# Kernel tuning notes

Measured on AMD Instinct MI355X. Metric: run time of the kernel, lower is better.

The kernel has to match this reference:

```python
import jax, jax.numpy as jnp
import numpy as np

N_IND, N_ORG, N_EXT = 1_000_000, 300_000, 100_000
F = 64
E = 1_000_000
# (src_type, dst_type) per relation, in HeteroConv dict order:
# txn: ind->ind, org->ind, ext->ind, ind->org, org->org, ext->org; role: ind->org;
# rev_txn: ind->ind, org->ind, ext->ind, ind->org, org->org, ext->org; rev_role: org->ind
RELS = [("ind","ind"),("org","ind"),("ext","ind"),("ind","org"),("org","org"),("ext","org"),
        ("ind","org"),("ind","ind"),("org","ind"),("ext","ind"),("ind","org"),("org","org"),
        ("ext","org"),("org","ind")]
N_OF = {"ind": N_IND, "org": N_ORG, "ext": N_EXT}


def setup_inputs() -> dict:
    key = jax.random.key(0)
    ks = jax.random.split(key, 8)
    x_ind = jax.random.normal(ks[0], (N_IND, F), dtype=jnp.float32)
    x_org = jax.random.normal(ks[1], (N_ORG, F), dtype=jnp.float32)
    x_ext = jax.random.normal(ks[2], (N_EXT, F), dtype=jnp.float32)
    Wl = jax.random.normal(ks[3], (14, F, 1), dtype=jnp.float32) * 0.1
    Wr = jax.random.normal(ks[4], (14, F, 1), dtype=jnp.float32) * 0.1
    b = jax.random.normal(ks[5], (14, 1), dtype=jnp.float32) * 0.1
    # Per-relation edge_index with src/dst ids in the correct node-count ranges.
    eis = []
    for r, (s, d) in enumerate(RELS):
        k1, k2 = jax.random.split(jax.random.fold_in(ks[6], r))
        src = jax.random.randint(k1, (E,), 0, N_OF[s], dtype=jnp.int32)
        dst = jax.random.randint(k2, (E,), 0, N_OF[d], dtype=jnp.int32)
        eis.append(jnp.stack([src, dst]))
    edge_index = jnp.stack(eis)  # [14, 2, E]
    return {"x_ind": x_ind, "x_org": x_org, "x_ext": x_ext,
            "Wl": Wl, "Wr": Wr, "b": b, "edge_index": edge_index}


def _segment_mean(feat, dst, num_segments):
    # PyG 'mean' aggr: zero for isolated dst nodes.
    s = jax.ops.segment_sum(feat, dst, num_segments=num_segments)          # [N_dst, F]
    c = jax.ops.segment_sum(jnp.ones((dst.shape[0], 1), feat.dtype), dst,
                            num_segments=num_segments)                      # [N_dst, 1]
    return s / jnp.maximum(c, 1.0)


def reference(x_ind, x_org, x_ext, Wl, Wr, b, edge_index):
    x = {"ind": x_ind, "org": x_org, "ext": x_ext}
    out = {"ind": jnp.zeros((N_IND, 1), x_ind.dtype),
           "org": jnp.zeros((N_ORG, 1), x_org.dtype)}
    for r, (s, d) in enumerate(RELS):
        src, dst = edge_index[r, 0], edge_index[r, 1]
        agg = _segment_mean(x[s][src], dst, N_OF[d])   # mean of neighbor feats [N_dst, F]
        # SAGEConv: lin_l(agg) + lin_r(x_dst); bias lives in lin_l. HeteroConv sums relations.
        out[d] = out[d] + agg @ Wl[r] + x[d] @ Wr[r] + b[r]
    pred_ind = jax.nn.sigmoid(out["ind"])[:, 0]
    pred_org = jax.nn.sigmoid(out["org"])[:, 0]
    return (pred_ind, pred_org)
```

## Files before the change

### kernel.cpp

```cpp
#include <hip/hip_runtime.h>
#include <hip/hip_fp16.h>

#define N_IND 1000000
#define N_ORG 300000
#define N_EXT 100000
#define F 64
#define E_PER 1000000
#define NREL 14

#define BW 1024
#define NB_IND 977
#define NB_ORG 293
#define NBKT 1270
#define NB_H 1024
#define CHUNK 4096
#define COLS_PER_REL 245
#define NCOL (NREL * COLS_PER_REL)
#define LAST_N (E_PER - (COLS_PER_REL - 1) * CHUNK)
#define COLS_PER_TYPE (7 * COLS_PER_REL)

#define FIX_SCALE 262144.0f
#define FIX_INV   3.814697265625e-6f

static const size_t OFF_PAY      = 0;
static const size_t OFF_CNTOFF   = 14049280;
static const size_t OFF_CNTOFF_T = 17561600;
static const size_t OFF_P_IND    = 21073920;
static const size_t OFF_P_ORG    = 23573920;
static const size_t OFF_P_EXT    = 24323920;
static const size_t OFF_BASE_IND = 24523920;
static const size_t OFF_BASE_ORG = 25523920;
static const size_t OFF_WM_IND   = 25823920;
static const size_t OFF_WM_ORG   = 25824304;
static const size_t OFF_WM_EXT   = 25824688;
static const size_t OFF_BSUM     = 25824944;

__global__ void prep_kernel(const float* __restrict__ Wl,
                            const float* __restrict__ Wr,
                            const float* __restrict__ b,
                            float* __restrict__ wm_ind,
                            float* __restrict__ wm_org,
                            float* __restrict__ wm_ext,
                            float* __restrict__ bsum) {
    int t = threadIdx.x;
    const int ind_wl[5] = {0, 3, 6, 7, 10};
    const int org_wl[5] = {1, 4, 8, 11, 13};
    const int ext_wl[4] = {2, 5, 9, 12};
    const int ind_r[7]  = {0, 1, 2, 7, 8, 9, 13};
    const int org_r[7]  = {3, 4, 5, 6, 10, 11, 12};
#pragma unroll
    for (int k = 0; k < 5; ++k) wm_ind[k * 64 + t] = Wl[ind_wl[k] * 64 + t];
#pragma unroll
    for (int k = 0; k < 5; ++k) wm_org[k * 64 + t] = Wl[org_wl[k] * 64 + t];
#pragma unroll
    for (int k = 0; k < 4; ++k) wm_ext[k * 64 + t] = Wl[ext_wl[k] * 64 + t];
    float si = 0.f, so = 0.f;
#pragma unroll
    for (int k = 0; k < 7; ++k) {
        si += Wr[ind_r[k] * 64 + t];
        so += Wr[org_r[k] * 64 + t];
    }
    wm_ind[5 * 64 + t] = si;
    wm_org[5 * 64 + t] = so;
    if (t == 0) {
        float bi = 0.f, bo = 0.f;
#pragma unroll
        for (int k = 0; k < 7; ++k) { bi += b[ind_r[k]]; bo += b[org_r[k]]; }
        bsum[0] = bi;
        bsum[1] = bo;
    }
}

template <int K, bool HASBASE>
__global__ __launch_bounds__(256) void proj_kernel(
    const float* __restrict__ x, int n,
    const float* __restrict__ wm,
    __half* __restrict__ p,
    float* __restrict__ base_out,
    const float* __restrict__ bsum) {
    int i = blockIdx.x * 256 + threadIdx.x;
    if (i >= n) return;
    const float4* xv = (const float4*)(x + (size_t)i * F);
    float acc[K];
#pragma unroll
    for (int k = 0; k < K; ++k) acc[k] = 0.f;
#pragma unroll
    for (int c = 0; c < 16; ++c) {
        float4 v = xv[c];
#pragma unroll
        for (int k = 0; k < K; ++k) {
            const float* w = wm + k * 64 + c * 4;
            acc[k] += v.x * w[0] + v.y * w[1] + v.z * w[2] + v.w * w[3];
        }
    }
    constexpr int NP = HASBASE ? K - 1 : K;
#pragma unroll
    for (int k = 0; k < NP; ++k) p[(size_t)k * n + i] = __float2half_rn(acc[k]);
    if (HASBASE) base_out[i] = acc[K - 1] + bsum[0];
}

__global__ __launch_bounds__(256, 7) void scatter_kernel(
    const int* __restrict__ ei,
    const unsigned short* __restrict__ p_ind,
    const unsigned short* __restrict__ p_org,
    const unsigned short* __restrict__ p_ext,
    unsigned* __restrict__ pay,
    unsigned* __restrict__ cntoff) {
    const int srcType[NREL] = {0,1,2,0,1,2,0,0,1,2,0,1,2,1};
    const int srcSlot[NREL] = {0,0,0,1,1,1,2,3,2,2,4,3,3,4};
    const int dstSlot[NREL] = {0,1,2,0,1,2,3,3,4,5,4,5,6,6};

    __shared__ unsigned h[NB_H];
    __shared__ unsigned stage[CHUNK];
    __shared__ unsigned wsum[4];

    const int t = threadIdx.x;
    const int lane = t & 63, wv = t >> 6;

    const int cid = blockIdx.x;
    const int r = cid / COLS_PER_REL;
    const int i = cid - r * COLS_PER_REL;
    const int n = (i == COLS_PER_REL - 1) ? LAST_N : CHUNK;
    const int n4 = n >> 2;
    const int* srcp = ei + ((size_t)r * 2 + 0) * E_PER + (size_t)i * CHUNK;
    const int* dstp = ei + ((size_t)r * 2 + 1) * E_PER + (size_t)i * CHUNK;
    const unsigned slotbits = (unsigned)dstSlot[r] << 10;
    const int st = srcType[r];
    const unsigned short* psrc =
        (st == 0) ? p_ind + (size_t)srcSlot[r] * N_IND :
        (st == 1) ? p_org + (size_t)srcSlot[r] * N_ORG :
                    p_ext + (size_t)srcSlot[r] * N_EXT;

#pragma unroll
    for (int j = 0; j < 4; ++j) h[t * 4 + j] = 0u;
    __syncthreads();
    const int4* dst4 = (const int4*)dstp;
    int4 dreg[4];
#pragma unroll
    for (int u = 0; u < 4; ++u) {
        int k = t + u * 256;
        if (k < n4) {
            int4 d = dst4[k];
            dreg[u] = d;
            atomicAdd(&h[d.x >> 10], 1u);
            atomicAdd(&h[d.y >> 10], 1u);
            atomicAdd(&h[d.z >> 10], 1u);
            atomicAdd(&h[d.w >> 10], 1u);
        }
    }
    __syncthreads();

    unsigned loc[4], s0 = 0;
#pragma unroll
    for (int j = 0; j < 4; ++j) { loc[j] = h[t * 4 + j]; s0 += loc[j]; }
    unsigned x = s0;
#pragma unroll
    for (int d = 1; d < 64; d <<= 1) {
        unsigned v = __shfl_up(x, d, 64);
        if (lane >= d) x += v;
    }
    if (lane == 63) wsum[wv] = x;
    __syncthreads();
    unsigned base = x - s0;
    for (int j = 0; j < wv; ++j) base += wsum[j];
    unsigned* co = cntoff + (size_t)cid * NB_H;
#pragma unroll
    for (int j = 0; j < 4; ++j) {
        co[t * 4 + j] = (base << 16) | loc[j];
        h[t * 4 + j] = base;
        base += loc[j];
    }
    __syncthreads();

    const int4* src4 = (const int4*)srcp;
#pragma unroll
    for (int u = 0; u < 4; ++u) {
        int k = t + u * 256;
        if (k < n4) {
            int4 s = src4[k];
            int4 d = dreg[u];
#pragma unroll
            for (int q = 0; q < 4; ++q) {
                int src = (q == 0) ? s.x : (q == 1) ? s.y : (q == 2) ? s.z : s.w;
                int dst = (q == 0) ? d.x : (q == 1) ? d.y : (q == 2) ? d.z : d.w;
                unsigned pvbits = psrc[src];
                unsigned word = (pvbits << 16) | slotbits | (unsigned)(dst & (BW - 1));
                unsigned pos = atomicAdd(&h[dst >> 10], 1u);
                stage[pos] = word;
            }
        }
    }
    __syncthreads();

    unsigned* payc = pay + (size_t)cid * CHUNK;
    for (int k = t; k < n; k += 256) payc[k] = stage[k];
}

__global__ __launch_bounds__(256) void transpose_kernel(
    const unsigned* __restrict__ in, unsigned* __restrict__ out) {
    __shared__ unsigned tb[32][33];
    const int c0 = blockIdx.x * 32;
    const int r0 = blockIdx.y * 32;
    const int tx = threadIdx.x & 31, ty = threadIdx.x >> 5;
#pragma unroll
    for (int j = 0; j < 32; j += 8) {
        int r = r0 + ty + j, c = c0 + tx;
        if (r < NCOL && c < NB_H) tb[ty + j][tx] = in[(size_t)r * NB_H + c];
    }
    __syncthreads();
#pragma unroll
    for (int j = 0; j < 32; j += 8) {
        int r = c0 + ty + j, c = r0 + tx;
        if (r < NB_H && c < NCOL) out[(size_t)r * NCOL + c] = tb[tx][ty + j];
    }
}

__global__ __launch_bounds__(256) void gather_kernel(
    const unsigned* __restrict__ pay,
    const unsigned* __restrict__ cntoffT,
    const float* __restrict__ base_ind,
    const float* __restrict__ base_org,
    float* __restrict__ out) {
    __shared__ unsigned acc[7 * BW];
    const int blk = blockIdx.x;
    const int t = threadIdx.x;
    for (int j = t; j < 7 * BW; j += 256) acc[j] = 0u;
    __syncthreads();

    const bool isInd = blk < NB_IND;
    const int b = isInd ? blk : blk - NB_IND;
    const int relsI[7] = {0, 1, 2, 7, 8, 9, 13};
    const int relsO[7] = {3, 4, 5, 6, 10, 11, 12};

    const unsigned* row = cntoffT + (size_t)b * NCOL;
    for (int j = t; j < COLS_PER_TYPE; j += 256) {
        int rl = j / COLS_PER_REL;
        int c = j - rl * COLS_PER_REL;
        int rel = isInd ? relsI[rl] : relsO[rl];
        int cid = rel * COLS_PER_REL + c;
        unsigned co = row[cid];
        unsigned cnt = co & 0xffffu;
        if (!cnt) continue;
        const unsigned* seg = pay + (size_t)cid * CHUNK + (co >> 16);
        for (unsigned e = 0; e < cnt; ++e) {
            unsigned w = seg[e];
            unsigned short hs = (unsigned short)(w >> 16);
            __half hh;
            __builtin_memcpy(&hh, &hs, 2);
            float pv = __half2float(hh);
            int fixed = (int)rintf(pv * FIX_SCALE);
            unsigned contrib = (1u << 26) + (unsigned)fixed;
            atomicAdd(&acc[((w >> 10) & 7u) * BW + (w & (BW - 1))], contrib);
        }
    }
    __syncthreads();

    const int nn = isInd ? N_IND : N_ORG;
    const float* basep = isInd ? base_ind : base_org;
    float* outp = isInd ? out : out + N_IND;
    for (int loc = t; loc < BW; loc += 256) {
        int g = b * BW + loc;
        if (g < nn) {
            float a = basep[g];
#pragma unroll
            for (int k = 0; k < 7; ++k) {
                unsigned w = acc[k * BW + loc];
                int s26 = ((int)(w << 6)) >> 6;
                unsigned c = (w - (unsigned)s26) >> 26;
                a += (float)s26 * FIX_INV / fmaxf((float)c, 1.0f);
            }
            outp[g] = 1.0f / (1.0f + __expf(-a));
        }
    }
}

extern "C" void kernel_launch(void* const* d_in, const int* in_sizes, int n_in,
                              void* d_out, int out_size, void* d_ws, size_t ws_size,
                              hipStream_t stream) {
    const float* x_ind = (const float*)d_in[0];
    const float* x_org = (const float*)d_in[1];
    const float* x_ext = (const float*)d_in[2];
    const float* Wl    = (const float*)d_in[3];
    const float* Wr    = (const float*)d_in[4];
    const float* b     = (const float*)d_in[5];
    const int*   ei    = (const int*)d_in[6];
    float* out = (float*)d_out;

    float* ws = (float*)d_ws;
    unsigned* pay      = (unsigned*)(ws + OFF_PAY);
    unsigned* cntoff   = (unsigned*)(ws + OFF_CNTOFF);
    unsigned* cntoffT  = (unsigned*)(ws + OFF_CNTOFF_T);
    __half* p_ind      = (__half*)(ws + OFF_P_IND);
    __half* p_org      = (__half*)(ws + OFF_P_ORG);
    __half* p_ext      = (__half*)(ws + OFF_P_EXT);
    float* base_ind    = ws + OFF_BASE_IND;
    float* base_org    = ws + OFF_BASE_ORG;
    float* wm_ind      = ws + OFF_WM_IND;
    float* wm_org      = ws + OFF_WM_ORG;
    float* wm_ext      = ws + OFF_WM_EXT;
    float* bsum        = ws + OFF_BSUM;

    prep_kernel<<<1, 64, 0, stream>>>(Wl, Wr, b, wm_ind, wm_org, wm_ext, bsum);

    proj_kernel<6, true><<<(N_IND + 255) / 256, 256, 0, stream>>>(
        x_ind, N_IND, wm_ind, p_ind, base_ind, bsum + 0);
    proj_kernel<6, true><<<(N_ORG + 255) / 256, 256, 0, stream>>>(
        x_org, N_ORG, wm_org, p_org, base_org, bsum + 1);
    proj_kernel<4, false><<<(N_EXT + 255) / 256, 256, 0, stream>>>(
        x_ext, N_EXT, wm_ext, p_ext, nullptr, bsum);

    scatter_kernel<<<NCOL, 256, 0, stream>>>(
        ei, (const unsigned short*)p_ind, (const unsigned short*)p_org,
        (const unsigned short*)p_ext, pay, cntoff);

    dim3 tgrid((NB_H + 31) / 32, (NCOL + 31) / 32);
    transpose_kernel<<<tgrid, 256, 0, stream>>>(cntoff, cntoffT);

    gather_kernel<<<NBKT, 256, 0, stream>>>(pay, cntoffT, base_ind, base_org, out);
}
```

Before: 288.5 us.

## Use narrower 256-node buckets for org destinations and split gather per type

```diff
diff --git a/kernel.cpp b/kernel.cpp
--- a/kernel.cpp
+++ b/kernel.cpp
@@ -8,11 +8,11 @@
 #define E_PER 1000000
 #define NREL 14
 
-#define BW 1024
+#define BW_IND 1024
+#define BW_ORG 256
 #define NB_IND 977
-#define NB_ORG 293
-#define NBKT 1270
-#define NB_H 1024
+#define NB_ORG 1172
+#define NB_HMAX 1280
 #define CHUNK 4096
 #define COLS_PER_REL 245
 #define NCOL (NREL * COLS_PER_REL)
@@ -24,16 +24,16 @@
 
 static const size_t OFF_PAY      = 0;
 static const size_t OFF_CNTOFF   = 14049280;
-static const size_t OFF_CNTOFF_T = 17561600;
-static const size_t OFF_P_IND    = 21073920;
-static const size_t OFF_P_ORG    = 23573920;
-static const size_t OFF_P_EXT    = 24323920;
-static const size_t OFF_BASE_IND = 24523920;
-static const size_t OFF_BASE_ORG = 25523920;
-static const size_t OFF_WM_IND   = 25823920;
-static const size_t OFF_WM_ORG   = 25824304;
-static const size_t OFF_WM_EXT   = 25824688;
-static const size_t OFF_BSUM     = 25824944;
+static const size_t OFF_CNTOFF_T = 18439680;
+static const size_t OFF_P_IND    = 22830080;
+static const size_t OFF_P_ORG    = 25330080;
+static const size_t OFF_P_EXT    = 26080080;
+static const size_t OFF_BASE_IND = 26280080;
+static const size_t OFF_BASE_ORG = 27280080;
+static const size_t OFF_WM_IND   = 27580080;
+static const size_t OFF_WM_ORG   = 27580464;
+static const size_t OFF_WM_EXT   = 27580848;
+static const size_t OFF_BSUM     = 27581104;
 
 __global__ void prep_kernel(const float* __restrict__ Wl,
                             const float* __restrict__ Wr,
@@ -109,22 +109,29 @@
     const int srcType[NREL] = {0,1,2,0,1,2,0,0,1,2,0,1,2,1};
     const int srcSlot[NREL] = {0,0,0,1,1,1,2,3,2,2,4,3,3,4};
     const int dstSlot[NREL] = {0,1,2,0,1,2,3,3,4,5,4,5,6,6};
-
-    __shared__ unsigned h[NB_H];
+    const int relsI[7] = {0, 1, 2, 7, 8, 9, 13};
+    const int relsO[7] = {3, 4, 5, 6, 10, 11, 12};
+
+    __shared__ unsigned h[NB_HMAX];
     __shared__ unsigned stage[CHUNK];
     __shared__ unsigned wsum[4];
 
     const int t = threadIdx.x;
     const int lane = t & 63, wv = t >> 6;
 
-    const int cid = blockIdx.x;
-    const int r = cid / COLS_PER_REL;
-    const int i = cid - r * COLS_PER_REL;
+    const bool isOrg = blockIdx.x >= COLS_PER_TYPE;
+    const int j0 = blockIdx.x - (isOrg ? COLS_PER_TYPE : 0);
+    const int rl = j0 / COLS_PER_REL;
+    const int i = j0 - rl * COLS_PER_REL;
+    const int r = (isOrg ? relsO : relsI)[rl];
+    const int shift = isOrg ? 8 : 10;
+    const unsigned lmask = (1u << shift) - 1u;
+    const int cid = r * COLS_PER_REL + i;
     const int n = (i == COLS_PER_REL - 1) ? LAST_N : CHUNK;
     const int n4 = n >> 2;
     const int* srcp = ei + ((size_t)r * 2 + 0) * E_PER + (size_t)i * CHUNK;
     const int* dstp = ei + ((size_t)r * 2 + 1) * E_PER + (size_t)i * CHUNK;
-    const unsigned slotbits = (unsigned)dstSlot[r] << 10;
+    const unsigned slotbits = (unsigned)dstSlot[r] << shift;
     const int st = srcType[r];
     const unsigned short* psrc =
         (st == 0) ? p_ind + (size_t)srcSlot[r] * N_IND :
@@ -132,7 +139,7 @@
                     p_ext + (size_t)srcSlot[r] * N_EXT;
 
 #pragma unroll
-    for (int j = 0; j < 4; ++j) h[t * 4 + j] = 0u;
+    for (int j = 0; j < 5; ++j) h[t * 5 + j] = 0u;
     __syncthreads();
     const int4* dst4 = (const int4*)dstp;
     int4 dreg[4];
@@ -142,17 +149,17 @@
         if (k < n4) {
             int4 d = dst4[k];
             dreg[u] = d;
-            atomicAdd(&h[d.x >> 10], 1u);
-            atomicAdd(&h[d.y >> 10], 1u);
-            atomicAdd(&h[d.z >> 10], 1u);
-            atomicAdd(&h[d.w >> 10], 1u);
-        }
-    }
-    __syncthreads();
-
-    unsigned loc[4], s0 = 0;
-#pragma unroll
-    for (int j = 0; j < 4; ++j) { loc[j] = h[t * 4 + j]; s0 += loc[j]; }
+            atomicAdd(&h[d.x >> shift], 1u);
+            atomicAdd(&h[d.y >> shift], 1u);
+            atomicAdd(&h[d.z >> shift], 1u);
+            atomicAdd(&h[d.w >> shift], 1u);
+        }
+    }
+    __syncthreads();
+
+    unsigned loc[5], s0 = 0;
+#pragma unroll
+    for (int j = 0; j < 5; ++j) { loc[j] = h[t * 5 + j]; s0 += loc[j]; }
     unsigned x = s0;
 #pragma unroll
     for (int d = 1; d < 64; d <<= 1) {
@@ -163,11 +170,11 @@
     __syncthreads();
     unsigned base = x - s0;
     for (int j = 0; j < wv; ++j) base += wsum[j];
-    unsigned* co = cntoff + (size_t)cid * NB_H;
-#pragma unroll
-    for (int j = 0; j < 4; ++j) {
-        co[t * 4 + j] = (base << 16) | loc[j];
-        h[t * 4 + j] = base;
+    unsigned* co = cntoff + (size_t)cid * NB_HMAX;
+#pragma unroll
+    for (int j = 0; j < 5; ++j) {
+        co[t * 5 + j] = (base << 16) | loc[j];
+        h[t * 5 + j] = base;
         base += loc[j];
     }
     __syncthreads();
@@ -184,16 +191,17 @@
                 int src = (q == 0) ? s.x : (q == 1) ? s.y : (q == 2) ? s.z : s.w;
                 int dst = (q == 0) ? d.x : (q == 1) ? d.y : (q == 2) ? d.z : d.w;
                 unsigned pvbits = psrc[src];
-                unsigned word = (pvbits << 16) | slotbits | (unsigned)(dst & (BW - 1));
-                unsigned pos = atomicAdd(&h[dst >> 10], 1u);
+                unsigned word = (pvbits << 16) | slotbits | ((unsigned)dst & lmask);
+                unsigned pos = atomicAdd(&h[dst >> shift], 1u);
                 stage[pos] = word;
             }
         }
     }
     __syncthreads();
 
-    unsigned* payc = pay + (size_t)cid * CHUNK;
-    for (int k = t; k < n; k += 256) payc[k] = stage[k];
+    uint4* payc4 = (uint4*)(pay + (size_t)cid * CHUNK);
+    const uint4* st4 = (const uint4*)stage;
+    for (int k = t; k < n4; k += 256) payc4[k] = st4[k];
 }
 
 __global__ __launch_bounds__(256) void transpose_kernel(
@@ -205,39 +213,38 @@
 #pragma unroll
     for (int j = 0; j < 32; j += 8) {
         int r = r0 + ty + j, c = c0 + tx;
-        if (r < NCOL && c < NB_H) tb[ty + j][tx] = in[(size_t)r * NB_H + c];
+        if (r < NCOL && c < NB_HMAX) tb[ty + j][tx] = in[(size_t)r * NB_HMAX + c];
     }
     __syncthreads();
 #pragma unroll
     for (int j = 0; j < 32; j += 8) {
         int r = c0 + ty + j, c = r0 + tx;
-        if (r < NB_H && c < NCOL) out[(size_t)r * NCOL + c] = tb[tx][ty + j];
-    }
-}
-
+        if (r < NB_HMAX && c < NCOL) out[(size_t)r * NCOL + c] = tb[tx][ty + j];
+    }
+}
+
+template <bool ISORG>
 __global__ __launch_bounds__(256) void gather_kernel(
     const unsigned* __restrict__ pay,
     const unsigned* __restrict__ cntoffT,
-    const float* __restrict__ base_ind,
-    const float* __restrict__ base_org,
-    float* __restrict__ out) {
-    __shared__ unsigned acc[7 * BW];
-    const int blk = blockIdx.x;
+    const float* __restrict__ base,
+    float* __restrict__ outp) {
+    constexpr int BWt = ISORG ? BW_ORG : BW_IND;
+    constexpr int shift = ISORG ? 8 : 10;
+    constexpr int nn = ISORG ? N_ORG : N_IND;
+    __shared__ unsigned acc[7 * BWt];
+    const int b = blockIdx.x;
     const int t = threadIdx.x;
-    for (int j = t; j < 7 * BW; j += 256) acc[j] = 0u;
-    __syncthreads();
-
-    const bool isInd = blk < NB_IND;
-    const int b = isInd ? blk : blk - NB_IND;
+    for (int j = t; j < 7 * BWt; j += 256) acc[j] = 0u;
+    __syncthreads();
+
     const int relsI[7] = {0, 1, 2, 7, 8, 9, 13};
     const int relsO[7] = {3, 4, 5, 6, 10, 11, 12};
-
     const unsigned* row = cntoffT + (size_t)b * NCOL;
     for (int j = t; j < COLS_PER_TYPE; j += 256) {
         int rl = j / COLS_PER_REL;
         int c = j - rl * COLS_PER_REL;
-        int rel = isInd ? relsI[rl] : relsO[rl];
-        int cid = rel * COLS_PER_REL + c;
+        int cid = (ISORG ? relsO[rl] : relsI[rl]) * COLS_PER_REL + c;
         unsigned co = row[cid];
         unsigned cnt = co & 0xffffu;
         if (!cnt) continue;
@@ -250,21 +257,18 @@
             float pv = __half2float(hh);
             int fixed = (int)rintf(pv * FIX_SCALE);
             unsigned contrib = (1u << 26) + (unsigned)fixed;
-            atomicAdd(&acc[((w >> 10) & 7u) * BW + (w & (BW - 1))], contrib);
-        }
-    }
-    __syncthreads();
-
-    const int nn = isInd ? N_IND : N_ORG;
-    const float* basep = isInd ? base_ind : base_org;
-    float* outp = isInd ? out : out + N_IND;
-    for (int loc = t; loc < BW; loc += 256) {
-        int g = b * BW + loc;
+            atomicAdd(&acc[((w >> shift) & 7u) * BWt + (w & (BWt - 1))], contrib);
+        }
+    }
+    __syncthreads();
+
+    for (int loc = t; loc < BWt; loc += 256) {
+        int g = b * BWt + loc;
         if (g < nn) {
-            float a = basep[g];
+            float a = base[g];
 #pragma unroll
             for (int k = 0; k < 7; ++k) {
-                unsigned w = acc[k * BW + loc];
+                unsigned w = acc[k * BWt + loc];
                 int s26 = ((int)(w << 6)) >> 6;
                 unsigned c = (w - (unsigned)s26) >> 26;
                 a += (float)s26 * FIX_INV / fmaxf((float)c, 1.0f);
@@ -309,12 +313,13 @@
     proj_kernel<4, false><<<(N_EXT + 255) / 256, 256, 0, stream>>>(
         x_ext, N_EXT, wm_ext, p_ext, nullptr, bsum);
 
-    scatter_kernel<<<NCOL, 256, 0, stream>>>(
+    scatter_kernel<<<2 * COLS_PER_TYPE, 256, 0, stream>>>(
         ei, (const unsigned short*)p_ind, (const unsigned short*)p_org,
         (const unsigned short*)p_ext, pay, cntoff);
 
-    dim3 tgrid((NB_H + 31) / 32, (NCOL + 31) / 32);
+    dim3 tgrid(NB_HMAX / 32, (NCOL + 31) / 32);
     transpose_kernel<<<tgrid, 256, 0, stream>>>(cntoff, cntoffT);
 
-    gather_kernel<<<NBKT, 256, 0, stream>>>(pay, cntoffT, base_ind, base_org, out);
-}
+    gather_kernel<false><<<NB_IND, 256, 0, stream>>>(pay, cntoffT, base_ind, out);
+    gather_kernel<true><<<NB_ORG, 256, 0, stream>>>(pay, cntoffT, base_org, out + N_IND);
+}
```

New measurement: 324.0 us. +12.3%, slower.

## Double scatter chunk size to 8192 edges with 512-thread blocks, reorder gather blocks

Applied to the files above, without the earlier changes.

```diff
diff --git a/kernel.cpp b/kernel.cpp
--- a/kernel.cpp
+++ b/kernel.cpp
@@ -13,27 +13,28 @@
 #define NB_ORG 293
 #define NBKT 1270
 #define NB_H 1024
-#define CHUNK 4096
-#define COLS_PER_REL 245
+#define CHUNK 8192
+#define COLS_PER_REL 123
 #define NCOL (NREL * COLS_PER_REL)
 #define LAST_N (E_PER - (COLS_PER_REL - 1) * CHUNK)
 #define COLS_PER_TYPE (7 * COLS_PER_REL)
+#define TSCAT 512
 
 #define FIX_SCALE 262144.0f
 #define FIX_INV   3.814697265625e-6f
 
 static const size_t OFF_PAY      = 0;
-static const size_t OFF_CNTOFF   = 14049280;
-static const size_t OFF_CNTOFF_T = 17561600;
-static const size_t OFF_P_IND    = 21073920;
-static const size_t OFF_P_ORG    = 23573920;
-static const size_t OFF_P_EXT    = 24323920;
-static const size_t OFF_BASE_IND = 24523920;
-static const size_t OFF_BASE_ORG = 25523920;
-static const size_t OFF_WM_IND   = 25823920;
-static const size_t OFF_WM_ORG   = 25824304;
-static const size_t OFF_WM_EXT   = 25824688;
-static const size_t OFF_BSUM     = 25824944;
+static const size_t OFF_CNTOFF   = 14106624;
+static const size_t OFF_CNTOFF_T = 15869952;
+static const size_t OFF_P_IND    = 17633280;
+static const size_t OFF_P_ORG    = 20133280;
+static const size_t OFF_P_EXT    = 20883280;
+static const size_t OFF_BASE_IND = 21083280;
+static const size_t OFF_BASE_ORG = 22083280;
+static const size_t OFF_WM_IND   = 22383280;
+static const size_t OFF_WM_ORG   = 22383664;
+static const size_t OFF_WM_EXT   = 22384048;
+static const size_t OFF_BSUM     = 22384304;
 
 __global__ void prep_kernel(const float* __restrict__ Wl,
                             const float* __restrict__ Wr,
@@ -99,7 +100,7 @@
     if (HASBASE) base_out[i] = acc[K - 1] + bsum[0];
 }
 
-__global__ __launch_bounds__(256, 7) void scatter_kernel(
+__global__ __launch_bounds__(TSCAT, 8) void scatter_kernel(
     const int* __restrict__ ei,
     const unsigned short* __restrict__ p_ind,
     const unsigned short* __restrict__ p_org,
@@ -112,7 +113,7 @@
 
     __shared__ unsigned h[NB_H];
     __shared__ unsigned stage[CHUNK];
-    __shared__ unsigned wsum[4];
+    __shared__ unsigned wsum[8];
 
     const int t = threadIdx.x;
     const int lane = t & 63, wv = t >> 6;
@@ -131,14 +132,14 @@
         (st == 1) ? p_org + (size_t)srcSlot[r] * N_ORG :
                     p_ext + (size_t)srcSlot[r] * N_EXT;
 
-#pragma unroll
-    for (int j = 0; j < 4; ++j) h[t * 4 + j] = 0u;
+    h[t * 2 + 0] = 0u;
+    h[t * 2 + 1] = 0u;
     __syncthreads();
     const int4* dst4 = (const int4*)dstp;
     int4 dreg[4];
 #pragma unroll
     for (int u = 0; u < 4; ++u) {
-        int k = t + u * 256;
+        int k = t + u * TSCAT;
         if (k < n4) {
             int4 d = dst4[k];
             dreg[u] = d;
@@ -150,9 +151,8 @@
     }
     __syncthreads();
 
-    unsigned loc[4], s0 = 0;
-#pragma unroll
-    for (int j = 0; j < 4; ++j) { loc[j] = h[t * 4 + j]; s0 += loc[j]; }
+    unsigned loc0 = h[t * 2 + 0], loc1 = h[t * 2 + 1];
+    unsigned s0 = loc0 + loc1;
     unsigned x = s0;
 #pragma unroll
     for (int d = 1; d < 64; d <<= 1) {
@@ -164,18 +164,17 @@
     unsigned base = x - s0;
     for (int j = 0; j < wv; ++j) base += wsum[j];
     unsigned* co = cntoff + (size_t)cid * NB_H;
-#pragma unroll
-    for (int j = 0; j < 4; ++j) {
-        co[t * 4 + j] = (base << 16) | loc[j];
-        h[t * 4 + j] = base;
-        base += loc[j];
-    }
+    co[t * 2 + 0] = (base << 16) | loc0;
+    h[t * 2 + 0] = base;
+    base += loc0;
+    co[t * 2 + 1] = (base << 16) | loc1;
+    h[t * 2 + 1] = base;
     __syncthreads();
 
     const int4* src4 = (const int4*)srcp;
 #pragma unroll
     for (int u = 0; u < 4; ++u) {
-        int k = t + u * 256;
+        int k = t + u * TSCAT;
         if (k < n4) {
             int4 s = src4[k];
             int4 d = dreg[u];
@@ -184,7 +183,7 @@
                 int src = (q == 0) ? s.x : (q == 1) ? s.y : (q == 2) ? s.z : s.w;
                 int dst = (q == 0) ? d.x : (q == 1) ? d.y : (q == 2) ? d.z : d.w;
                 unsigned pvbits = psrc[src];
-                unsigned word = (pvbits << 16) | slotbits | (unsigned)(dst & (BW - 1));
+                unsigned word = (pvbits << 16) | slotbits | ((unsigned)dst & (BW - 1));
                 unsigned pos = atomicAdd(&h[dst >> 10], 1u);
                 stage[pos] = word;
             }
@@ -192,8 +191,9 @@
     }
     __syncthreads();
 
-    unsigned* payc = pay + (size_t)cid * CHUNK;
-    for (int k = t; k < n; k += 256) payc[k] = stage[k];
+    uint4* payc4 = (uint4*)(pay + (size_t)cid * CHUNK);
+    const uint4* st4 = (const uint4*)stage;
+    for (int k = t; k < n4; k += TSCAT) payc4[k] = st4[k];
 }
 
 __global__ __launch_bounds__(256) void transpose_kernel(
@@ -227,8 +227,8 @@
     for (int j = t; j < 7 * BW; j += 256) acc[j] = 0u;
     __syncthreads();
 
-    const bool isInd = blk < NB_IND;
-    const int b = isInd ? blk : blk - NB_IND;
+    const bool isOrg = blk < NB_ORG;
+    const int b = isOrg ? blk : blk - NB_ORG;
     const int relsI[7] = {0, 1, 2, 7, 8, 9, 13};
     const int relsO[7] = {3, 4, 5, 6, 10, 11, 12};
 
@@ -236,8 +236,7 @@
     for (int j = t; j < COLS_PER_TYPE; j += 256) {
         int rl = j / COLS_PER_REL;
         int c = j - rl * COLS_PER_REL;
-        int rel = isInd ? relsI[rl] : relsO[rl];
-        int cid = rel * COLS_PER_REL + c;
+        int cid = (isOrg ? relsO[rl] : relsI[rl]) * COLS_PER_REL + c;
         unsigned co = row[cid];
         unsigned cnt = co & 0xffffu;
         if (!cnt) continue;
@@ -255,9 +254,9 @@
     }
     __syncthreads();
 
-    const int nn = isInd ? N_IND : N_ORG;
-    const float* basep = isInd ? base_ind : base_org;
-    float* outp = isInd ? out : out + N_IND;
+    const int nn = isOrg ? N_ORG : N_IND;
+    const float* basep = isOrg ? base_org : base_ind;
+    float* outp = isOrg ? out + N_IND : out;
     for (int loc = t; loc < BW; loc += 256) {
         int g = b * BW + loc;
         if (g < nn) {
@@ -309,11 +308,11 @@
     proj_kernel<4, false><<<(N_EXT + 255) / 256, 256, 0, stream>>>(
         x_ext, N_EXT, wm_ext, p_ext, nullptr, bsum);
 
-    scatter_kernel<<<NCOL, 256, 0, stream>>>(
+    scatter_kernel<<<NCOL, TSCAT, 0, stream>>>(
         ei, (const unsigned short*)p_ind, (const unsigned short*)p_org,
         (const unsigned short*)p_ext, pay, cntoff);
 
-    dim3 tgrid((NB_H + 31) / 32, (NCOL + 31) / 32);
+    dim3 tgrid(NB_H / 32, (NCOL + 31) / 32);
     transpose_kernel<<<tgrid, 256, 0, stream>>>(cntoff, cntoffT);
 
     gather_kernel<<<NBKT, 256, 0, stream>>>(pay, cntoffT, base_ind, base_org, out);
```

After: 265.9 us. -7.8%, faster.
